# Kernel tuning notes

Measured on AMD Instinct MI355X. Metric: run time of the kernel, lower is better.

## Reference

```python
import jax, jax.numpy as jnp
import numpy as np

N_PARTS, P_IDS, K_SAMP, D_FEAT = 62, 64, 8, 256
MARGIN = 0.2


def setup_inputs() -> dict:
    key = jax.random.key(0)
    k1, = jax.random.split(key, 1)
    m = P_IDS * K_SAMP
    feature = jax.random.normal(k1, (N_PARTS, m, D_FEAT), dtype=jnp.float32)
    # structured labels: P ids, K samples each, identical across parts
    # (required by the masked_select(...).view(n, m, -1) contract)
    lab = jnp.repeat(jnp.arange(P_IDS, dtype=jnp.int64), K_SAMP)
    label = jnp.tile(lab[None, :], (N_PARTS, 1))
    view = jnp.zeros((N_PARTS, m), dtype=jnp.int64)  # unused by forward
    return {"feature": feature, "label": label, "view": view}


def _mine_indices(label):
    # label rows are identical across parts; counts per anchor are constant.
    lab = np.asarray(label[0])
    m = lab.shape[0]
    same = lab[None, :] == lab[:, None]            # [m, m] bool
    k = int(same[0].sum())
    pos_idx = np.nonzero(same)[1].reshape(m, k)     # row-major == masked_select order
    neg_idx = np.nonzero(~same)[1].reshape(m, m - k)
    return jnp.asarray(pos_idx), jnp.asarray(neg_idx)


def _batch_dist(x):
    # x: [n, m, d] -> pairwise euclidean dist [n, m, m]
    x2 = jnp.sum(x * x, axis=2)                              # [n, m]
    d2 = x2[:, :, None] + x2[:, None, :] - 2.0 * jnp.einsum('nmd,nkd->nmk', x, x)
    d2 = jnp.maximum(d2, 0.0)
    # safe sqrt: forward identical to sqrt(relu(d2)); avoids NaN grad at 0
    return jnp.where(d2 > 0, jnp.sqrt(jnp.where(d2 > 0, d2, 1.0)), 0.0)


def reference(feature, label, view):
    n, m, _ = feature.shape
    pos_idx, neg_idx = _mine_indices(label)

    dist = _batch_dist(feature)                 # [n, m, m]
    mean_dist = dist.mean(axis=(1, 2))          # [n]

    rows = jnp.arange(m)[:, None]
    hp = dist[:, rows, pos_idx]                 # [n, m, K]   same-label dists
    hn = dist[:, rows, neg_idx]                 # [n, m, m-K] diff-label dists

    hard = jax.nn.relu(MARGIN + hp.max(axis=2) - hn.min(axis=2))  # [n, m]
    hard_loss_metric_mean = hard.mean(axis=1)                      # [n]

    full = jax.nn.relu(MARGIN + hp[:, :, :, None] - hn[:, :, None, :])  # [n,m,K,m-K]
    full = full.reshape(n, -1)
    full_sum = full.sum(axis=1)
    full_num = (full != 0).sum(axis=1).astype(feature.dtype)
    full_loss_metric_mean = jnp.where(full_num == 0, 0.0,
                                      full_sum / jnp.maximum(full_num, 1.0))
    return (full_loss_metric_mean, hard_loss_metric_mean, mean_dist, full_num)
```

## Files before the change

kernel.cpp:

```cpp
#include <hip/hip_runtime.h>
#include <math.h>

#define NPART 62
#define M 512
#define D 256
#define KSAMP 8
#define MARGIN 0.2f
#define NT 256
#define BKK 32
#define NKSTEP (D / BKK)

typedef __attribute__((ext_vector_type(8))) short bf16x8;
typedef __attribute__((ext_vector_type(4))) float f32x4;

__device__ __forceinline__ unsigned bf16_rne(float f) {
    unsigned u = __builtin_bit_cast(unsigned, f);
    return (u + 0x7FFFu + ((u >> 16) & 1u)) >> 16;
}

__global__ __launch_bounds__(NT, 2) void triplet_main(
    const float* __restrict__ feat, const int* __restrict__ label,
    float* __restrict__ ws)
{
    __shared__ bf16x8 hiS[M * 4];
    __shared__ bf16x8 loS[M * 4];
    __shared__ float  x2s[M];
    __shared__ int    labsS[M];
    __shared__ __align__(16) float hpL[64 * 8];
    __shared__ float  hnw[64 * 4];

    const int t    = threadIdx.x;
    const int lane = t & 63;
    const int w    = t >> 6;
    const int lr   = lane & 15;
    const int h    = lane >> 4;

    const int d_ = blockIdx.x;
    const int s  = (d_ & 7) * 62 + (d_ >> 3);
    const int n  = s >> 3;
    const int bx = s & 7;
    const int R0 = bx * 64;
    const float* F = feat + (size_t)n * (M * D);

    labsS[t]       = label[n * M + t];
    labsS[t + 256] = label[n * M + t + 256];

    float x2q[8];
#pragma unroll
    for (int i = 0; i < 8; ++i) x2q[i] = 0.f;

    f32x4 acc[4][8];
    const f32x4 zero4 = {0.f, 0.f, 0.f, 0.f};
#pragma unroll
    for (int a = 0; a < 4; ++a)
#pragma unroll
        for (int b = 0; b < 8; ++b) acc[a][b] = zero4;

    int aIdx[4], bIdx[8];
#pragma unroll
    for (int rb = 0; rb < 4; ++rb) {
        const int row = R0 + rb * 16 + lr;
        aIdx[rb] = row * 4 + (h ^ ((row >> 1) & 3));
    }
#pragma unroll
    for (int cb = 0; cb < 8; ++cb) {
        const int row = w * 128 + cb * 16 + lr;
        bIdx[cb] = row * 4 + (h ^ ((row >> 1) & 3));
    }
    int sRowA[8], sDstA[8];
#pragma unroll
    for (int it = 0; it < 8; ++it) {
        const int idx = t + 256 * it;
        const int row = idx >> 2, qq = idx & 3;
        sRowA[it] = row;
        sDstA[it] = row * 4 + (qq ^ ((row >> 1) & 3));
    }
    const int qoff = (t & 3) * 8;

    for (int kc = 0; kc < NKSTEP; ++kc) {
        const int k0 = kc * BKK;
        __syncthreads();
#pragma unroll
        for (int it = 0; it < 8; ++it) {
            const float* src = F + (size_t)sRowA[it] * D + k0 + qoff;
            const float4 v0 = *(const float4*)src;
            const float4 v1 = *(const float4*)(src + 4);
            const float v[8] = {v0.x, v0.y, v0.z, v0.w, v1.x, v1.y, v1.z, v1.w};
            bf16x8 h8, l8;
#pragma unroll
            for (int e = 0; e < 8; ++e) {
                const float f = v[e];
                const unsigned hr = bf16_rne(f);
                const float hf = __builtin_bit_cast(float, hr << 16);
                h8[e] = (short)hr;
                l8[e] = (short)bf16_rne(f - hf);
                x2q[it] += f * f;
            }
            hiS[sDstA[it]] = h8;
            loS[sDstA[it]] = l8;
        }
        __syncthreads();

        bf16x8 ah[4], al[4];
#pragma unroll
        for (int rb = 0; rb < 4; ++rb) { ah[rb] = hiS[aIdx[rb]]; al[rb] = loS[aIdx[rb]]; }
#pragma unroll
        for (int cb = 0; cb < 8; ++cb) {
            const bf16x8 bh = hiS[bIdx[cb]];
            const bf16x8 bl = loS[bIdx[cb]];
#pragma unroll
            for (int rb = 0; rb < 4; ++rb) {
                acc[rb][cb] = __builtin_amdgcn_mfma_f32_16x16x32_bf16(ah[rb], bh, acc[rb][cb], 0, 0, 0);
                acc[rb][cb] = __builtin_amdgcn_mfma_f32_16x16x32_bf16(al[rb], bh, acc[rb][cb], 0, 0, 0);
                acc[rb][cb] = __builtin_amdgcn_mfma_f32_16x16x32_bf16(ah[rb], bl, acc[rb][cb], 0, 0, 0);
            }
        }
    }

#pragma unroll
    for (int it = 0; it < 8; ++it) {
        float x = x2q[it];
        x += __shfl_xor(x, 1);
        x += __shfl_xor(x, 2);
        if ((t & 3) == 0) x2s[sRowA[it]] = x;
    }
    __syncthreads();

    float x2r[4][4];
    int   labr_[4][4];
#pragma unroll
    for (int rb = 0; rb < 4; ++rb)
#pragma unroll
        for (int q = 0; q < 4; ++q) {
            const int gi = R0 + rb * 16 + h * 4 + q;
            x2r[rb][q]  = x2s[gi];
            labr_[rb][q] = labsS[gi];
        }
    float x2c[8];
    int   labc[8];
#pragma unroll
    for (int cb = 0; cb < 8; ++cb) {
        const int cj = w * 128 + cb * 16 + lr;
        x2c[cb] = x2s[cj];
        labc[cb] = labsS[cj];
    }

    float mdsum = 0.f;
#pragma unroll
    for (int rb = 0; rb < 4; ++rb)
#pragma unroll
        for (int cb = 0; cb < 8; ++cb) {
            f32x4 a = acc[rb][cb];
#pragma unroll
            for (int q = 0; q < 4; ++q) {
                const float d2 = x2r[rb][q] + x2c[cb] - 2.f * a[q];
                const float dd = (d2 > 0.f) ? sqrtf(d2) : 0.f;
                a[q] = dd;
                mdsum += dd;
                if (labc[cb] == labr_[rb][q])
                    hpL[(rb * 16 + h * 4 + q) * 8 + (lane & 7)] = dd;
            }
            acc[rb][cb] = a;
        }
    __syncthreads();

    float fsum = 0.f, fcnt = 0.f;
#pragma unroll
    for (int rb = 0; rb < 4; ++rb)
#pragma unroll
        for (int q = 0; q < 4; ++q) {
            const int rl   = rb * 16 + h * 4 + q;
            const int labi = labr_[rb][q];
            const float4 hp0 = *(const float4*)&hpL[rl * 8];
            const float4 hp1 = *(const float4*)&hpL[rl * 8 + 4];
            const float mhp[8] = {MARGIN + hp0.x, MARGIN + hp0.y, MARGIN + hp0.z, MARGIN + hp0.w,
                                  MARGIN + hp1.x, MARGIN + hp1.y, MARGIN + hp1.z, MARGIN + hp1.w};
            float hn = 3.0e38f;
#pragma unroll
            for (int cb = 0; cb < 8; ++cb) {
                if (labc[cb] != labi) {
                    const float dd = acc[rb][cb][q];
                    hn = fminf(hn, dd);
#pragma unroll
                    for (int p = 0; p < 8; ++p) {
                        const float vv = mhp[p] - dd;
                        fsum += fmaxf(vv, 0.f);
                        fcnt += (vv > 0.f) ? 1.f : 0.f;
                    }
                }
            }
            hn = fminf(hn, __shfl_xor(hn, 1));
            hn = fminf(hn, __shfl_xor(hn, 2));
            hn = fminf(hn, __shfl_xor(hn, 4));
            hn = fminf(hn, __shfl_xor(hn, 8));
            if (lr == 0) hnw[rl * 4 + w] = hn;
        }

#pragma unroll
    for (int o = 32; o > 0; o >>= 1) {
        fsum  += __shfl_xor(fsum, o);
        fcnt  += __shfl_xor(fcnt, o);
        mdsum += __shfl_xor(mdsum, o);
    }
    if (lane == 0) {
        atomicAdd(&ws[n * 4 + 0], fsum);
        atomicAdd(&ws[n * 4 + 1], fcnt);
        atomicAdd(&ws[n * 4 + 3], mdsum);
    }
    __syncthreads();

    if (t < 64) {
        const float hn = fminf(fminf(hnw[t * 4 + 0], hnw[t * 4 + 1]),
                               fminf(hnw[t * 4 + 2], hnw[t * 4 + 3]));
        float hm = hpL[t * 8];
#pragma unroll
        for (int p = 1; p < 8; ++p) hm = fmaxf(hm, hpL[t * 8 + p]);
        float hd = MARGIN + hm - hn;
        hd = (hd > 0.f) ? hd : 0.f;
#pragma unroll
        for (int o = 32; o > 0; o >>= 1) hd += __shfl_xor(hd, o);
        if (t == 0) atomicAdd(&ws[n * 4 + 2], hd);
    }
}

__global__ void triplet_finalize(const float* __restrict__ ws,
                                 float* __restrict__ out)
{
    const int i = threadIdx.x;
    if (i < NPART) {
        const float fs = ws[i * 4 + 0];
        const float fc = ws[i * 4 + 1];
        const float hs = ws[i * 4 + 2];
        const float ds = ws[i * 4 + 3];
        out[i]             = (fc == 0.f) ? 0.f : fs / fmaxf(fc, 1.f);
        out[NPART + i]     = hs / (float)M;
        out[2 * NPART + i] = ds / ((float)M * (float)M);
        out[3 * NPART + i] = fc;
    }
}

extern "C" void kernel_launch(void* const* d_in, const int* in_sizes, int n_in,
                              void* d_out, int out_size, void* d_ws, size_t ws_size,
                              hipStream_t stream)
{
    (void)in_sizes; (void)n_in; (void)out_size; (void)ws_size;
    const float* feat  = (const float*)d_in[0];
    const int*   label = (const int*)d_in[1];
    float*       ws    = (float*)d_ws;

    hipMemsetAsync(ws, 0, NPART * 4 * sizeof(float), stream);
    triplet_main<<<dim3(NPART * 8), NT, 0, stream>>>(feat, label, ws);
    triplet_finalize<<<1, 64, 0, stream>>>(ws, (float*)d_out);
}
```

Baseline: 84.68 us.

## Precompute bf16 hi/lo split in prep kernel, double-buffer LDS in larger-tile main kernel

Adds a prep kernel that computes row norms and splits the fp32 features into bf16 hi/lo halves once, written in a pre-swizzled layout to workspace. The main kernel now uses 512 threads with 128-row tiles over 248 blocks, loads the preconverted bf16 data, and double-buffers LDS so the next K-chunk's global loads overlap the MFMAs. This removes the per-block redundant fp32-to-bf16 conversion and halves the number of times each part's features are re-read. In exchange it adds an extra launch and a write/read of the bf16 copies through global memory, and uses more LDS per block. The old kernel remains as a fallback when the workspace is too small.

After: 90.69 us. +7.1%, slower.

```diff
diff --git a/kernel.cpp b/kernel.cpp
--- a/kernel.cpp
+++ b/kernel.cpp
@@ -6,11 +6,9 @@
 #define D 256
 #define KSAMP 8
 #define MARGIN 0.2f
-#define NT 256
-#define BKK 32
-#define NKSTEP (D / BKK)
 
 typedef __attribute__((ext_vector_type(8))) short bf16x8;
+typedef __attribute__((ext_vector_type(4))) short s16x4;
 typedef __attribute__((ext_vector_type(4))) float f32x4;
 
 __device__ __forceinline__ unsigned bf16_rne(float f) {
@@ -18,7 +16,244 @@
     return (u + 0x7FFFu + ((u >> 16) & 1u)) >> 16;
 }
 
-__global__ __launch_bounds__(NT, 2) void triplet_main(
+__global__ __launch_bounds__(256) void triplet_prep(
+    const float* __restrict__ feat, float* __restrict__ x2_ws,
+    short* __restrict__ hi_ws, short* __restrict__ lo_ws)
+{
+    const int t  = threadIdx.x;
+    const int l  = t & 63;
+    const int w  = t >> 6;
+    const int rg = blockIdx.x * 4 + w;
+    const int row = rg & (M - 1);
+
+    const float4 v = *(const float4*)(feat + (size_t)rg * D + l * 4);
+    float x2 = v.x * v.x + v.y * v.y + v.z * v.z + v.w * v.w;
+    const float vf[4] = {v.x, v.y, v.z, v.w};
+    s16x4 hs, ls;
+#pragma unroll
+    for (int e = 0; e < 4; ++e) {
+        const unsigned hr = bf16_rne(vf[e]);
+        hs[e] = (short)hr;
+        ls[e] = (short)bf16_rne(vf[e] - __builtin_bit_cast(float, hr << 16));
+    }
+    const int kc = l >> 3;
+    const int g  = (l >> 1) & 3;
+    const int sw = (row ^ (row >> 2)) & 3;
+    const size_t base = (size_t)rg * D + kc * 32 + (g ^ sw) * 8 + (l & 1) * 4;
+    *(s16x4*)(hi_ws + base) = hs;
+    *(s16x4*)(lo_ws + base) = ls;
+#pragma unroll
+    for (int o = 32; o > 0; o >>= 1) x2 += __shfl_xor(x2, o);
+    if (l == 0) x2_ws[rg] = x2;
+}
+
+__global__ __launch_bounds__(512, 2) void triplet_main(
+    const short* __restrict__ hi_ws, const short* __restrict__ lo_ws,
+    const float* __restrict__ x2_ws, const int* __restrict__ label,
+    float* __restrict__ ws)
+{
+    __shared__ short hiA[2 * M * 32];
+    __shared__ short loA[2 * M * 32];
+    __shared__ float x2s[M];
+    __shared__ int   labsS[M];
+    __shared__ __align__(16) float hpL[128 * 8];
+    __shared__ float hnw[128 * 4];
+
+    const int t    = threadIdx.x;
+    const int lane = t & 63;
+    const int w    = t >> 6;
+    const int lr   = lane & 15;
+    const int h    = lane >> 4;
+
+    const int d_ = blockIdx.x;
+    const int s  = (d_ & 7) * 31 + (d_ >> 3);
+    const int n  = s >> 2;
+    const int bx = s & 3;
+    const int R0 = bx * 128;
+    const int rw = (w >> 2) * 64;
+    const int cw = (w & 3) * 128;
+
+    labsS[t] = label[n * M + t];
+    x2s[t]   = x2_ws[n * M + t];
+
+    size_t gbase[4];
+    int    ldst[4];
+#pragma unroll
+    for (int it = 0; it < 4; ++it) {
+        const int c   = w * 4 + it;
+        const int row = c * 16 + (lane >> 2);
+        const int g   = lane & 3;
+        gbase[it] = ((size_t)n * M + row) * D + g * 8;
+        ldst[it]  = c * 512 + lane * 8;
+    }
+    int aOff[4], bOff[8];
+#pragma unroll
+    for (int rb = 0; rb < 4; ++rb) {
+        const int row = R0 + rw + rb * 16 + lr;
+        aOff[rb] = row * 32 + ((h ^ ((row ^ (row >> 2)) & 3)) * 8);
+    }
+#pragma unroll
+    for (int cb = 0; cb < 8; ++cb) {
+        const int row = cw + cb * 16 + lr;
+        bOff[cb] = row * 32 + ((h ^ ((row ^ (row >> 2)) & 3)) * 8);
+    }
+
+    f32x4 acc[4][8];
+    const f32x4 zero4 = {0.f, 0.f, 0.f, 0.f};
+#pragma unroll
+    for (int a = 0; a < 4; ++a)
+#pragma unroll
+        for (int bq = 0; bq < 8; ++bq) acc[a][bq] = zero4;
+
+    bf16x8 sgh[4], sgl[4];
+#pragma unroll
+    for (int it = 0; it < 4; ++it) {
+        sgh[it] = *(const bf16x8*)(hi_ws + gbase[it]);
+        sgl[it] = *(const bf16x8*)(lo_ws + gbase[it]);
+    }
+#pragma unroll
+    for (int it = 0; it < 4; ++it) {
+        *(bf16x8*)&hiA[ldst[it]] = sgh[it];
+        *(bf16x8*)&loA[ldst[it]] = sgl[it];
+    }
+    __syncthreads();
+
+    int b = 0;
+    for (int kc = 0; kc < 8; ++kc) {
+        if (kc < 7) {
+            const size_t kb = (size_t)(kc + 1) * 32;
+#pragma unroll
+            for (int it = 0; it < 4; ++it) {
+                sgh[it] = *(const bf16x8*)(hi_ws + gbase[it] + kb);
+                sgl[it] = *(const bf16x8*)(lo_ws + gbase[it] + kb);
+            }
+        }
+        const int bo = b * (M * 32);
+        bf16x8 ah[4], al[4];
+#pragma unroll
+        for (int rb = 0; rb < 4; ++rb) {
+            ah[rb] = *(const bf16x8*)&hiA[bo + aOff[rb]];
+            al[rb] = *(const bf16x8*)&loA[bo + aOff[rb]];
+        }
+#pragma unroll
+        for (int cb = 0; cb < 8; ++cb) {
+            const bf16x8 bh = *(const bf16x8*)&hiA[bo + bOff[cb]];
+            const bf16x8 bl = *(const bf16x8*)&loA[bo + bOff[cb]];
+#pragma unroll
+            for (int rb = 0; rb < 4; ++rb) {
+                acc[rb][cb] = __builtin_amdgcn_mfma_f32_16x16x32_bf16(ah[rb], bh, acc[rb][cb], 0, 0, 0);
+                acc[rb][cb] = __builtin_amdgcn_mfma_f32_16x16x32_bf16(al[rb], bh, acc[rb][cb], 0, 0, 0);
+                acc[rb][cb] = __builtin_amdgcn_mfma_f32_16x16x32_bf16(ah[rb], bl, acc[rb][cb], 0, 0, 0);
+            }
+        }
+        if (kc < 7) {
+            const int to = (b ^ 1) * (M * 32);
+#pragma unroll
+            for (int it = 0; it < 4; ++it) {
+                *(bf16x8*)&hiA[to + ldst[it]] = sgh[it];
+                *(bf16x8*)&loA[to + ldst[it]] = sgl[it];
+            }
+        }
+        __syncthreads();
+        b ^= 1;
+    }
+
+    float x2r[4][4]; int labr_[4][4];
+#pragma unroll
+    for (int rb = 0; rb < 4; ++rb)
+#pragma unroll
+        for (int q = 0; q < 4; ++q) {
+            const int ri = R0 + rw + rb * 16 + h * 4 + q;
+            x2r[rb][q]   = x2s[ri];
+            labr_[rb][q] = labsS[ri];
+        }
+    float x2c[8]; int labc[8];
+#pragma unroll
+    for (int cb = 0; cb < 8; ++cb) {
+        const int cj = cw + cb * 16 + lr;
+        x2c[cb] = x2s[cj];
+        labc[cb] = labsS[cj];
+    }
+
+    float mdsum = 0.f;
+#pragma unroll
+    for (int rb = 0; rb < 4; ++rb)
+#pragma unroll
+        for (int cb = 0; cb < 8; ++cb) {
+            f32x4 a = acc[rb][cb];
+#pragma unroll
+            for (int q = 0; q < 4; ++q) {
+                const float d2 = x2r[rb][q] + x2c[cb] - 2.f * a[q];
+                const float dd = (d2 > 0.f) ? sqrtf(d2) : 0.f;
+                a[q] = dd;
+                mdsum += dd;
+                if (labc[cb] == labr_[rb][q])
+                    hpL[(rw + rb * 16 + h * 4 + q) * 8 + (lane & 7)] = dd;
+            }
+            acc[rb][cb] = a;
+        }
+    __syncthreads();
+
+    float fsum = 0.f, fcnt = 0.f;
+#pragma unroll
+    for (int rb = 0; rb < 4; ++rb)
+#pragma unroll
+        for (int q = 0; q < 4; ++q) {
+            const int rl   = rw + rb * 16 + h * 4 + q;
+            const int labi = labr_[rb][q];
+            const float4 hp0 = *(const float4*)&hpL[rl * 8];
+            const float4 hp1 = *(const float4*)&hpL[rl * 8 + 4];
+            const float mhp[8] = {MARGIN + hp0.x, MARGIN + hp0.y, MARGIN + hp0.z, MARGIN + hp0.w,
+                                  MARGIN + hp1.x, MARGIN + hp1.y, MARGIN + hp1.z, MARGIN + hp1.w};
+            float hn = 3.0e38f;
+#pragma unroll
+            for (int cb = 0; cb < 8; ++cb) {
+                if (labc[cb] != labi) {
+                    const float dd = acc[rb][cb][q];
+                    hn = fminf(hn, dd);
+#pragma unroll
+                    for (int p = 0; p < 8; ++p) {
+                        const float vv = mhp[p] - dd;
+                        fsum += fmaxf(vv, 0.f);
+                        fcnt += (vv > 0.f) ? 1.f : 0.f;
+                    }
+                }
+            }
+            hn = fminf(hn, __shfl_xor(hn, 1));
+            hn = fminf(hn, __shfl_xor(hn, 2));
+            hn = fminf(hn, __shfl_xor(hn, 4));
+            hn = fminf(hn, __shfl_xor(hn, 8));
+            if (lr == 0) hnw[rl * 4 + (w & 3)] = hn;
+        }
+
+#pragma unroll
+    for (int o = 32; o > 0; o >>= 1) {
+        fsum  += __shfl_xor(fsum, o);
+        fcnt  += __shfl_xor(fcnt, o);
+        mdsum += __shfl_xor(mdsum, o);
+    }
+    if (lane == 0) {
+        atomicAdd(&ws[n * 4 + 0], fsum);
+        atomicAdd(&ws[n * 4 + 1], fcnt);
+        atomicAdd(&ws[n * 4 + 3], mdsum);
+    }
+    __syncthreads();
+
+    if (t < 128) {
+        const float hn = fminf(fminf(hnw[t * 4 + 0], hnw[t * 4 + 1]),
+                               fminf(hnw[t * 4 + 2], hnw[t * 4 + 3]));
+        float hm = hpL[t * 8];
+#pragma unroll
+        for (int p = 1; p < 8; ++p) hm = fmaxf(hm, hpL[t * 8 + p]);
+        float hd = MARGIN + hm - hn;
+        hd = (hd > 0.f) ? hd : 0.f;
+#pragma unroll
+        for (int o = 32; o > 0; o >>= 1) hd += __shfl_xor(hd, o);
+        if (lane == 0) atomicAdd(&ws[n * 4 + 2], hd);
+    }
+}
+
+__global__ __launch_bounds__(256, 2) void triplet_main_fb(
     const float* __restrict__ feat, const int* __restrict__ label,
     float* __restrict__ ws)
 {
@@ -54,7 +289,7 @@
 #pragma unroll
     for (int a = 0; a < 4; ++a)
 #pragma unroll
-        for (int b = 0; b < 8; ++b) acc[a][b] = zero4;
+        for (int bq = 0; bq < 8; ++bq) acc[a][bq] = zero4;
 
     int aIdx[4], bIdx[8];
 #pragma unroll
@@ -77,8 +312,8 @@
     }
     const int qoff = (t & 3) * 8;
 
-    for (int kc = 0; kc < NKSTEP; ++kc) {
-        const int k0 = kc * BKK;
+    for (int kc = 0; kc < 8; ++kc) {
+        const int k0 = kc * 32;
         __syncthreads();
 #pragma unroll
         for (int it = 0; it < 8; ++it) {
@@ -126,18 +361,16 @@
     }
     __syncthreads();
 
-    float x2r[4][4];
-    int   labr_[4][4];
+    float x2r[4][4]; int labr_[4][4];
 #pragma unroll
     for (int rb = 0; rb < 4; ++rb)
 #pragma unroll
         for (int q = 0; q < 4; ++q) {
             const int gi = R0 + rb * 16 + h * 4 + q;
-            x2r[rb][q]  = x2s[gi];
+            x2r[rb][q]   = x2s[gi];
             labr_[rb][q] = labsS[gi];
         }
-    float x2c[8];
-    int   labc[8];
+    float x2c[8]; int labc[8];
 #pragma unroll
     for (int cb = 0; cb < 8; ++cb) {
         const int cj = w * 128 + cb * 16 + lr;
@@ -243,12 +476,24 @@
                               void* d_out, int out_size, void* d_ws, size_t ws_size,
                               hipStream_t stream)
 {
-    (void)in_sizes; (void)n_in; (void)out_size; (void)ws_size;
+    (void)in_sizes; (void)n_in; (void)out_size;
     const float* feat  = (const float*)d_in[0];
     const int*   label = (const int*)d_in[1];
     float*       ws    = (float*)d_ws;
 
+    const size_t HI_OFF = 131072;
+    const size_t LO_OFF = HI_OFF + (size_t)NPART * M * D * 2;
+    const size_t NEEDED = LO_OFF + (size_t)NPART * M * D * 2;
+
     hipMemsetAsync(ws, 0, NPART * 4 * sizeof(float), stream);
-    triplet_main<<<dim3(NPART * 8), NT, 0, stream>>>(feat, label, ws);
+    if (ws_size >= NEEDED) {
+        float* x2_ws = (float*)((char*)d_ws + 4096);
+        short* hi_ws = (short*)((char*)d_ws + HI_OFF);
+        short* lo_ws = (short*)((char*)d_ws + LO_OFF);
+        triplet_prep<<<dim3(NPART * M / 4), 256, 0, stream>>>(feat, x2_ws, hi_ws, lo_ws);
+        triplet_main<<<dim3(248), 512, 0, stream>>>(hi_ws, lo_ws, x2_ws, label, ws);
+    } else {
+        triplet_main_fb<<<dim3(NPART * 8), 256, 0, stream>>>(feat, label, ws);
+    }
     triplet_finalize<<<1, 64, 0, stream>>>(ws, (float*)d_out);
 }
```
